# Optimization experiments

Measured on AMD Instinct MI355X. Metric: run time of the kernel, lower is better.

Reference implementation:

```python
import jax, jax.numpy as jnp
import numpy as np

B, D, S = 8, 128, 4096

def setup_inputs() -> dict:
    key = jax.random.key(0)
    ks = jax.random.split(key, 7)
    sd = 1.0 / np.sqrt(D)
    return {
        "x": jax.random.normal(ks[0], (B, D, S), dtype=jnp.float32),
        "Wq": jax.random.normal(ks[1], (D, D), dtype=jnp.float32) * sd,
        "bq": jax.random.normal(ks[2], (D,), dtype=jnp.float32) * sd,
        "Wk": jax.random.normal(ks[3], (D, D), dtype=jnp.float32) * sd,
        "bk": jax.random.normal(ks[4], (D,), dtype=jnp.float32) * sd,
        "Wv": jax.random.normal(ks[5], (D, D), dtype=jnp.float32) * sd,
        "bv": jax.random.normal(ks[6], (D,), dtype=jnp.float32) * sd,
    }

def reference(x, Wq, bq, Wk, bk, Wv, bv):
    # x: (B, D, S) -> (B, S, D)
    xt = jnp.transpose(x, (0, 2, 1))
    scale = jnp.asarray(D, xt.dtype) ** 0.5
    # torch Linear: y = x @ W.T + b
    Q = jnp.einsum('bsd,ed->bse', xt, Wq) + bq
    K = jnp.einsum('bsd,ed->bse', xt, Wk) + bk
    V = jnp.einsum('bsd,ed->bse', xt, Wv) + bv
    scores = jnp.einsum('bqd,bkd->bqk', Q, K) / scale  # (B, S, S)
    attn = jax.nn.softmax(scores, axis=-1)
    attended = jnp.einsum('bqk,bkd->bqd', attn, V)
    out = xt + attended  # residual
    return jnp.transpose(out, (0, 2, 1))  # back to (B, D, S)
```

## Files before the change

### kernel.cpp

```cpp
#include <hip/hip_runtime.h>
#include <hip/hip_bf16.h>

#define B_ 8
#define D_ 128
#define S_ 4096

typedef short short8 __attribute__((ext_vector_type(8)));
typedef float f32x4  __attribute__((ext_vector_type(4)));
typedef float f32x16 __attribute__((ext_vector_type(16)));
typedef unsigned int uint;
typedef uint uint4v __attribute__((ext_vector_type(4)));

#define EXP2F(x) exp2f(x)

__device__ __forceinline__ short f2bf(float f) {
    __hip_bfloat16 h = __float2bfloat16(f);
    return *reinterpret_cast<short*>(&h);
}

__device__ __forceinline__ uint cvtpk(float lo, float hi) {
    uint r;
    asm("v_cvt_pk_bf16_f32 %0, %1, %2" : "=v"(r) : "v"(lo), "v"(hi));
    return r;
}

__device__ __forceinline__ void gload16(const void* g, void* l) {
    __builtin_amdgcn_global_load_lds(
        (const __attribute__((address_space(1))) void*)g,
        (__attribute__((address_space(3))) void*)l, 16, 0, 0);
}

__global__ __launch_bounds__(256) void wpack_kernel(
    const float* __restrict__ Wq, const float* __restrict__ Wk,
    const float* __restrict__ Wv, short* __restrict__ Wf)
{
    int g = blockIdx.x * 256 + threadIdx.x;
    int lane = g & 63, kc = (g >> 6) & 3, n = (g >> 8) & 7, wm = g >> 11;
    const float* W = (wm == 0) ? Wq : (wm == 1) ? Wk : Wv;
    int row = n * 16 + (lane & 15);
    int col = kc * 32 + (lane >> 4) * 8;
    short8 o;
    #pragma unroll
    for (int j = 0; j < 8; ++j) o[j] = f2bf(W[row * 128 + col + j]);
    *((short8*)Wf + g) = o;
}

__global__ __launch_bounds__(256) void qkv_kernel(
    const float* __restrict__ x, const short* __restrict__ Wf,
    const float* __restrict__ bq, const float* __restrict__ bk,
    const float* __restrict__ bv,
    short* __restrict__ Qo, short* __restrict__ Ko, short* __restrict__ Vo)
{
    __shared__ float xt[64 * 132];
    const int b  = blockIdx.y;
    const int s0 = blockIdx.x * 64;
    const int t  = threadIdx.x;
    const int w    = t >> 6;
    const int lane = t & 63;
    const int lr   = lane & 15;
    const int lg   = lane >> 4;

    const float* xb = x + (size_t)b * D_ * S_;
    #pragma unroll
    for (int it = 0; it < 32; ++it) {
        int d = it * 4 + (t >> 6);
        int s = t & 63;
        xt[s * 132 + d] = xb[(size_t)d * S_ + s0 + s];
    }
    __syncthreads();

    short8 xtf[4];
    {
        const float* base = &xt[(w * 16 + lr) * 132 + lg * 8];
        #pragma unroll
        for (int kc = 0; kc < 4; ++kc) {
            float4 a = *(const float4*)(base + kc * 32);
            float4 c = *(const float4*)(base + kc * 32 + 4);
            short8 f;
            f[0] = f2bf(a.x); f[1] = f2bf(a.y); f[2] = f2bf(a.z); f[3] = f2bf(a.w);
            f[4] = f2bf(c.x); f[5] = f2bf(c.y); f[6] = f2bf(c.z); f[7] = f2bf(c.w);
            xtf[kc] = f;
        }
    }

    const float qs = 0.08838834764831845f * 1.4426950408889634f;
    const short8* W8 = (const short8*)Wf;
    const size_t bSD = (size_t)b * S_ * D_;
    const size_t bDS = (size_t)b * D_ * S_;

    #pragma unroll
    for (int n = 0; n < 8; ++n) {
        f32x4 aq = (f32x4){0.f, 0.f, 0.f, 0.f};
        f32x4 ak = (f32x4){0.f, 0.f, 0.f, 0.f};
        f32x4 av = (f32x4){0.f, 0.f, 0.f, 0.f};
        #pragma unroll
        for (int kc = 0; kc < 4; ++kc) {
            short8 wq = W8[(      n * 4 + kc) * 64 + lane];
            short8 wk = W8[(32  + n * 4 + kc) * 64 + lane];
            short8 wv = W8[(64  + n * 4 + kc) * 64 + lane];
            aq = __builtin_amdgcn_mfma_f32_16x16x32_bf16(xtf[kc], wq, aq, 0, 0, 0);
            ak = __builtin_amdgcn_mfma_f32_16x16x32_bf16(xtf[kc], wk, ak, 0, 0, 0);
            av = __builtin_amdgcn_mfma_f32_16x16x32_bf16(wv, xtf[kc], av, 0, 0, 0);
        }
        int e = n * 16 + lr;
        float bqe = bq[e], bke = bk[e];
        #pragma unroll
        for (int r = 0; r < 4; ++r) {
            size_t off = (bSD + (size_t)(s0 + w * 16 + lg * 4 + r) * D_) + e;
            Qo[off] = f2bf((aq[r] + bqe) * qs);
            Ko[off] = f2bf(ak[r] + bke);
        }
        #pragma unroll
        for (int r = 0; r < 4; ++r) {
            int ev = n * 16 + lg * 4 + r;
            Vo[bDS + (size_t)ev * S_ + s0 + w * 16 + lr] = f2bf(av[r] + bv[ev]);
        }
    }
}

__global__ __launch_bounds__(512, 2) void attn_kernel(
    const short* __restrict__ Q, const short* __restrict__ K,
    const short* __restrict__ Vt, const float* __restrict__ x,
    float* __restrict__ out)
{
    extern __shared__ __align__(16) char smem[];
    const int lin = blockIdx.x;
    const int b   = lin & 7;
    const int q0  = (lin >> 3) * 128;
    const int t    = threadIdx.x;
    const int w    = t >> 6;
    const int lane = t & 63;
    const int q    = lane & 31;
    const int hi   = lane >> 5;
    const int half = w >> 2;
    const int ww   = w & 3;

    const size_t bSD = (size_t)b * S_ * D_;

    short8 qf[8];
    {
        const short* Qrow = Q + bSD + (size_t)(q0 + ww * 32 + q) * D_ + hi * 8;
        #pragma unroll
        for (int c = 0; c < 8; ++c)
            qf[c] = *(const short8*)(Qrow + c * 16);
    }

    f32x16 o[4];
    #pragma unroll
    for (int dt = 0; dt < 4; ++dt)
        #pragma unroll
        for (int i = 0; i < 16; ++i) o[dt][i] = 0.f;
    float m = -1e30f, lsum = 0.f;

    const short* Kb = K + bSD;
    const short* Vb = Vt + (size_t)b * D_ * S_;
    const int ktbase = half * 32;

    auto stage = [&](int kt, int buf) {
        const short* Kg = Kb + (size_t)(ktbase + kt) * 64 * D_;
        const short* Vg = Vb + (size_t)(ktbase + kt) * 64;
        char* Kd = smem + buf * 65536 + half * 32768;
        char* Vd = Kd + 16384;
        #pragma unroll
        for (int i = 0; i < 4; ++i) {
            int ki = ww * 4 + i;
            int r  = ki * 4 + (lane >> 4);
            gload16(Kg + r * D_ + (((lane & 15) ^ (r & 7)) * 8), Kd + ki * 1024);
        }
        #pragma unroll
        for (int i = 0; i < 4; ++i) {
            int vi = ww * 4 + i;
            int r  = vi * 8 + (lane >> 3);
            gload16(Vg + (size_t)r * S_ + (((lane & 7) ^ (lane >> 3)) * 8),
                    Vd + vi * 1024);
        }
    };

    stage(0, 0);
    __syncthreads();
    int cur = 0;

    for (int kt = 0; kt < 32; ++kt) {
        if (kt + 1 < 32) stage(kt + 1, cur ^ 1);

        const char* Kh = smem + cur * 65536 + half * 32768;
        const char* Vh = Kh + 16384;

        f32x16 acc[2];
        #pragma unroll
        for (int n = 0; n < 2; ++n)
            #pragma unroll
            for (int i = 0; i < 16; ++i) acc[n][i] = 0.f;
        #pragma unroll
        for (int c = 0; c < 8; ++c) {
            #pragma unroll
            for (int n = 0; n < 2; ++n) {
                int row = n * 32 + q;
                short8 kf = *(const short8*)(Kh + row * 256
                              + (((c * 2 + hi) ^ (q & 7)) * 16));
                acc[n] = __builtin_amdgcn_mfma_f32_32x32x16_bf16(kf, qf[c], acc[n], 0, 0, 0);
            }
        }

        float tm = acc[0][0];
        #pragma unroll
        for (int n = 0; n < 2; ++n)
            #pragma unroll
            for (int r = 0; r < 16; ++r) tm = fmaxf(tm, acc[n][r]);
        tm = fmaxf(tm, __shfl_xor(tm, 32));
        if (!__all(tm <= m + 8.f)) {
            float mn   = fmaxf(m, tm);
            float corr = EXP2F(m - mn);
            m = mn; lsum *= corr;
            #pragma unroll
            for (int dt = 0; dt < 4; ++dt)
                #pragma unroll
                for (int r = 0; r < 16; ++r) o[dt][r] *= corr;
        }
        float ps = 0.f;
        #pragma unroll
        for (int n = 0; n < 2; ++n)
            #pragma unroll
            for (int r = 0; r < 16; ++r) {
                float e = EXP2F(acc[n][r] - m);
                acc[n][r] = e; ps += e;
            }
        ps += __shfl_xor(ps, 32);
        lsum += ps;

        short8 pf[4];
        #pragma unroll
        for (int kc = 0; kc < 4; ++kc) {
            int n = kc >> 1, c1 = (kc & 1) * 8;
            uint W0 = cvtpk(acc[n][c1 + 0], acc[n][c1 + 1]);
            uint W1 = cvtpk(acc[n][c1 + 2], acc[n][c1 + 3]);
            uint W2 = cvtpk(acc[n][c1 + 4], acc[n][c1 + 5]);
            uint W3 = cvtpk(acc[n][c1 + 6], acc[n][c1 + 7]);
            uint S0 = __shfl_xor(W0, 32);
            uint S1 = __shfl_xor(W1, 32);
            uint S2 = __shfl_xor(W2, 32);
            uint S3 = __shfl_xor(W3, 32);
            uint4v pw;
            pw.x = hi ? S2 : W0;
            pw.y = hi ? S3 : W1;
            pw.z = hi ? W2 : S0;
            pw.w = hi ? W3 : S1;
            pf[kc] = *reinterpret_cast<short8*>(&pw);
        }

        __builtin_amdgcn_s_setprio(1);
        #pragma unroll
        for (int kc = 0; kc < 4; ++kc) {
            #pragma unroll
            for (int dt = 0; dt < 4; ++dt) {
                int row = dt * 32 + q;
                short8 vf = *(const short8*)(Vh + row * 128
                              + (((kc * 2 + hi) ^ (q & 7)) * 16));
                o[dt] = __builtin_amdgcn_mfma_f32_32x32x16_bf16(vf, pf[kc], o[dt], 0, 0, 0);
            }
        }
        __builtin_amdgcn_s_setprio(0);

        __syncthreads();
        cur ^= 1;
    }

    if (half == 1) {
        float* obuf = (float*)(smem + ww * 16384);
        #pragma unroll
        for (int dt = 0; dt < 4; ++dt)
            #pragma unroll
            for (int r = 0; r < 16; ++r) {
                int dl = dt * 32 + (r & 3) + 8 * (r >> 2) + 4 * hi;
                obuf[dl * 32 + q] = o[dt][r];
            }
        if (hi == 0) {
            float* ml = (float*)(smem + 65536 + ww * 256);
            ml[q * 2]     = m;
            ml[q * 2 + 1] = lsum;
        }
    }
    __syncthreads();
    if (half == 0) {
        const float* obuf = (const float*)(smem + ww * 16384);
        const float* ml   = (const float*)(smem + 65536 + ww * 256);
        float m2 = ml[q * 2], l2 = ml[q * 2 + 1];
        float M  = fmaxf(m, m2);
        float c1 = EXP2F(m - M), c2 = EXP2F(m2 - M);
        float inv = 1.0f / (lsum * c1 + l2 * c2);
        const float* xb = x   + (size_t)b * D_ * S_;
        float*       ob = out + (size_t)b * D_ * S_;
        int s = q0 + ww * 32 + q;
        #pragma unroll
        for (int dt = 0; dt < 4; ++dt)
            #pragma unroll
            for (int r = 0; r < 16; ++r) {
                int dl = dt * 32 + (r & 3) + 8 * (r >> 2) + 4 * hi;
                float val = (o[dt][r] * c1 + obuf[dl * 32 + q] * c2) * inv;
                size_t g = (size_t)dl * S_ + s;
                ob[g] = xb[g] + val;
            }
    }
}

extern "C" void kernel_launch(void* const* d_in, const int* in_sizes, int n_in,
                              void* d_out, int out_size, void* d_ws, size_t ws_size,
                              hipStream_t stream) {
    const float* x  = (const float*)d_in[0];
    const float* Wq = (const float*)d_in[1];
    const float* bq = (const float*)d_in[2];
    const float* Wk = (const float*)d_in[3];
    const float* bk = (const float*)d_in[4];
    const float* Wv = (const float*)d_in[5];
    const float* bv = (const float*)d_in[6];
    float* out = (float*)d_out;

    size_t n = (size_t)B_ * S_ * D_;
    short* Qw = (short*)d_ws;
    short* Kw = Qw + n;
    short* Vw = Kw + n;
    short* Wf = (short*)d_out;

    wpack_kernel<<<24, 256, 0, stream>>>(Wq, Wk, Wv, Wf);

    dim3 grid(S_ / 64, B_);
    qkv_kernel<<<grid, 256, 0, stream>>>(x, Wf, bq, bk, bv, Qw, Kw, Vw);

    int smemB = 131072;
    (void)hipFuncSetAttribute((const void*)attn_kernel,
                              hipFuncAttributeMaxDynamicSharedMemorySize, smemB);
    attn_kernel<<<256, 512, smemB, stream>>>(Qw, Kw, Vw, x, out);
}
```

Measured before the change: 123.7 us.

## Split attention into 4-way KV partitions with smaller query tiles and direct V loads

Each block now handles 64 queries and splits the key range four ways across wave pairs, processing 32 keys per step instead of 64. V is read straight from global memory instead of being staged through LDS, which halves LDS use and raises the launch-bounds occupancy target. The P-fragment transpose uses v_permlane32_swap instead of shuffles. A four-way softmax merge runs through LDS at the end. The risks are uncoalesced global V reads, more synchronization per unit of work, and greater register pressure.

```diff
diff --git a/kernel.cpp b/kernel.cpp
--- a/kernel.cpp
+++ b/kernel.cpp
@@ -118,7 +118,7 @@
     }
 }
 
-__global__ __launch_bounds__(512, 2) void attn_kernel(
+__global__ __launch_bounds__(512, 4) void attn_kernel(
     const short* __restrict__ Q, const short* __restrict__ K,
     const short* __restrict__ Vt, const float* __restrict__ x,
     float* __restrict__ out)
@@ -126,14 +126,14 @@
     extern __shared__ __align__(16) char smem[];
     const int lin = blockIdx.x;
     const int b   = lin & 7;
-    const int q0  = (lin >> 3) * 128;
+    const int q0  = (lin >> 3) * 64;
     const int t    = threadIdx.x;
     const int w    = t >> 6;
     const int lane = t & 63;
     const int q    = lane & 31;
     const int hi   = lane >> 5;
-    const int half = w >> 2;
-    const int ww   = w & 3;
+    const int qr   = w >> 1;
+    const int ww   = w & 1;
 
     const size_t bSD = (size_t)b * S_ * D_;
 
@@ -154,26 +154,17 @@
 
     const short* Kb = K + bSD;
     const short* Vb = Vt + (size_t)b * D_ * S_;
-    const int ktbase = half * 32;
+    const int kvbase = qr * 1024;
 
     auto stage = [&](int kt, int buf) {
-        const short* Kg = Kb + (size_t)(ktbase + kt) * 64 * D_;
-        const short* Vg = Vb + (size_t)(ktbase + kt) * 64;
-        char* Kd = smem + buf * 65536 + half * 32768;
-        char* Vd = Kd + 16384;
+        const short* Kg = Kb + (size_t)(kvbase + kt * 32) * D_;
+        char* Kd = smem + buf * 32768 + qr * 8192;
         #pragma unroll
         for (int i = 0; i < 4; ++i) {
             int ki = ww * 4 + i;
             int r  = ki * 4 + (lane >> 4);
             gload16(Kg + r * D_ + (((lane & 15) ^ (r & 7)) * 8), Kd + ki * 1024);
         }
-        #pragma unroll
-        for (int i = 0; i < 4; ++i) {
-            int vi = ww * 4 + i;
-            int r  = vi * 8 + (lane >> 3);
-            gload16(Vg + (size_t)r * S_ + (((lane & 7) ^ (lane >> 3)) * 8),
-                    Vd + vi * 1024);
-        }
     };
 
     stage(0, 0);
@@ -183,30 +174,28 @@
     for (int kt = 0; kt < 32; ++kt) {
         if (kt + 1 < 32) stage(kt + 1, cur ^ 1);
 
-        const char* Kh = smem + cur * 65536 + half * 32768;
-        const char* Vh = Kh + 16384;
-
-        f32x16 acc[2];
-        #pragma unroll
-        for (int n = 0; n < 2; ++n)
-            #pragma unroll
-            for (int i = 0; i < 16; ++i) acc[n][i] = 0.f;
+        const char* Kh = smem + cur * 32768 + qr * 8192;
+
+        f32x16 acc;
+        #pragma unroll
+        for (int i = 0; i < 16; ++i) acc[i] = 0.f;
+        __builtin_amdgcn_s_setprio(1);
         #pragma unroll
         for (int c = 0; c < 8; ++c) {
-            #pragma unroll
-            for (int n = 0; n < 2; ++n) {
-                int row = n * 32 + q;
-                short8 kf = *(const short8*)(Kh + row * 256
-                              + (((c * 2 + hi) ^ (q & 7)) * 16));
-                acc[n] = __builtin_amdgcn_mfma_f32_32x32x16_bf16(kf, qf[c], acc[n], 0, 0, 0);
-            }
-        }
-
-        float tm = acc[0][0];
-        #pragma unroll
-        for (int n = 0; n < 2; ++n)
-            #pragma unroll
-            for (int r = 0; r < 16; ++r) tm = fmaxf(tm, acc[n][r]);
+            short8 kf = *(const short8*)(Kh + q * 256
+                          + (((c * 2 + hi) ^ (q & 7)) * 16));
+            acc = __builtin_amdgcn_mfma_f32_32x32x16_bf16(kf, qf[c], acc, 0, 0, 0);
+        }
+        __builtin_amdgcn_s_setprio(0);
+
+        float t0 = fmaxf(acc[0],  acc[1]),  t1 = fmaxf(acc[2],  acc[3]);
+        float t2 = fmaxf(acc[4],  acc[5]),  t3 = fmaxf(acc[6],  acc[7]);
+        float t4 = fmaxf(acc[8],  acc[9]),  t5 = fmaxf(acc[10], acc[11]);
+        float t6 = fmaxf(acc[12], acc[13]), t7 = fmaxf(acc[14], acc[15]);
+        float ta = fmaxf(fmaxf(t0, t1), t2);
+        float tb = fmaxf(fmaxf(t3, t4), t5);
+        float tc = fmaxf(t6, t7);
+        float tm = fmaxf(fmaxf(ta, tb), tc);
         tm = fmaxf(tm, __shfl_xor(tm, 32));
         if (!__all(tm <= m + 8.f)) {
             float mn   = fmaxf(m, tm);
@@ -217,77 +206,107 @@
                 #pragma unroll
                 for (int r = 0; r < 16; ++r) o[dt][r] *= corr;
         }
-        float ps = 0.f;
-        #pragma unroll
-        for (int n = 0; n < 2; ++n)
-            #pragma unroll
-            for (int r = 0; r < 16; ++r) {
-                float e = EXP2F(acc[n][r] - m);
-                acc[n][r] = e; ps += e;
-            }
+        #pragma unroll
+        for (int r = 0; r < 16; ++r) acc[r] = EXP2F(acc[r] - m);
+        float s0 = (acc[0] + acc[1]) + (acc[2] + acc[3]);
+        float s1 = (acc[4] + acc[5]) + (acc[6] + acc[7]);
+        float s2 = (acc[8] + acc[9]) + (acc[10] + acc[11]);
+        float s3 = (acc[12] + acc[13]) + (acc[14] + acc[15]);
+        float ps = (s0 + s1) + (s2 + s3);
         ps += __shfl_xor(ps, 32);
         lsum += ps;
 
-        short8 pf[4];
-        #pragma unroll
-        for (int kc = 0; kc < 4; ++kc) {
-            int n = kc >> 1, c1 = (kc & 1) * 8;
-            uint W0 = cvtpk(acc[n][c1 + 0], acc[n][c1 + 1]);
-            uint W1 = cvtpk(acc[n][c1 + 2], acc[n][c1 + 3]);
-            uint W2 = cvtpk(acc[n][c1 + 4], acc[n][c1 + 5]);
-            uint W3 = cvtpk(acc[n][c1 + 6], acc[n][c1 + 7]);
-            uint S0 = __shfl_xor(W0, 32);
-            uint S1 = __shfl_xor(W1, 32);
-            uint S2 = __shfl_xor(W2, 32);
-            uint S3 = __shfl_xor(W3, 32);
+        short8 pf[2];
+        #pragma unroll
+        for (int kc = 0; kc < 2; ++kc) {
+            int c1 = kc * 8;
+            uint W0 = cvtpk(acc[c1 + 0], acc[c1 + 1]);
+            uint W1 = cvtpk(acc[c1 + 2], acc[c1 + 3]);
+            uint W2 = cvtpk(acc[c1 + 4], acc[c1 + 5]);
+            uint W3 = cvtpk(acc[c1 + 6], acc[c1 + 7]);
+            asm("v_permlane32_swap_b32 %0, %1" : "+v"(W0), "+v"(W2));
+            asm("v_permlane32_swap_b32 %0, %1" : "+v"(W1), "+v"(W3));
             uint4v pw;
-            pw.x = hi ? S2 : W0;
-            pw.y = hi ? S3 : W1;
-            pw.z = hi ? W2 : S0;
-            pw.w = hi ? W3 : S1;
+            pw.x = W0;
+            pw.y = W1;
+            pw.z = W2;
+            pw.w = W3;
             pf[kc] = *reinterpret_cast<short8*>(&pw);
         }
 
+        const short* Vg = Vb + kvbase + kt * 32 + hi * 8;
         __builtin_amdgcn_s_setprio(1);
         #pragma unroll
-        for (int kc = 0; kc < 4; ++kc) {
+        for (int kc = 0; kc < 2; ++kc)
             #pragma unroll
             for (int dt = 0; dt < 4; ++dt) {
-                int row = dt * 32 + q;
-                short8 vf = *(const short8*)(Vh + row * 128
-                              + (((kc * 2 + hi) ^ (q & 7)) * 16));
+                short8 vf = *(const short8*)(Vg + (size_t)(dt * 32 + q) * S_
+                                             + kc * 16);
                 o[dt] = __builtin_amdgcn_mfma_f32_32x32x16_bf16(vf, pf[kc], o[dt], 0, 0, 0);
             }
-        }
         __builtin_amdgcn_s_setprio(0);
 
         __syncthreads();
         cur ^= 1;
     }
 
-    if (half == 1) {
-        float* obuf = (float*)(smem + ww * 16384);
+    float2* ml = (float2*)(smem + 65536);
+    if (hi == 0) {
+        float2 v2; v2.x = m; v2.y = lsum;
+        ml[(ww * 4 + qr) * 32 + q] = v2;
+    }
+    __syncthreads();
+    float M = -1e30f;
+    float mx[4], ly[4];
+    #pragma unroll
+    for (int i = 0; i < 4; ++i) {
+        float2 v2 = ml[(ww * 4 + i) * 32 + q];
+        mx[i] = v2.x; ly[i] = v2.y;
+        M = fmaxf(M, mx[i]);
+    }
+    float L = 0.f;
+    #pragma unroll
+    for (int i = 0; i < 4; ++i) L += ly[i] * EXP2F(mx[i] - M);
+    float cf = EXP2F(m - M);
+    #pragma unroll
+    for (int dt = 0; dt < 4; ++dt)
+        #pragma unroll
+        for (int r = 0; r < 16; ++r) o[dt][r] *= cf;
+
+    float* buf01 = (float*)smem + ww * 4096;
+    float* buf23 = (float*)smem + 8192 + ww * 4096;
+    if (qr == 1 || qr == 3) {
+        float* bw = (qr == 1) ? buf01 : buf23;
         #pragma unroll
         for (int dt = 0; dt < 4; ++dt)
             #pragma unroll
             for (int r = 0; r < 16; ++r) {
                 int dl = dt * 32 + (r & 3) + 8 * (r >> 2) + 4 * hi;
-                obuf[dl * 32 + q] = o[dt][r];
-            }
-        if (hi == 0) {
-            float* ml = (float*)(smem + 65536 + ww * 256);
-            ml[q * 2]     = m;
-            ml[q * 2 + 1] = lsum;
-        }
-    }
-    __syncthreads();
-    if (half == 0) {
-        const float* obuf = (const float*)(smem + ww * 16384);
-        const float* ml   = (const float*)(smem + 65536 + ww * 256);
-        float m2 = ml[q * 2], l2 = ml[q * 2 + 1];
-        float M  = fmaxf(m, m2);
-        float c1 = EXP2F(m - M), c2 = EXP2F(m2 - M);
-        float inv = 1.0f / (lsum * c1 + l2 * c2);
+                bw[dl * 32 + q] = o[dt][r];
+            }
+    }
+    __syncthreads();
+    if (qr == 0) {
+        #pragma unroll
+        for (int dt = 0; dt < 4; ++dt)
+            #pragma unroll
+            for (int r = 0; r < 16; ++r) {
+                int dl = dt * 32 + (r & 3) + 8 * (r >> 2) + 4 * hi;
+                o[dt][r] += buf01[dl * 32 + q];
+            }
+    } else if (qr == 2) {
+        #pragma unroll
+        for (int dt = 0; dt < 4; ++dt)
+            #pragma unroll
+            for (int r = 0; r < 16; ++r) {
+                int dl = dt * 32 + (r & 3) + 8 * (r >> 2) + 4 * hi;
+                o[dt][r] += buf23[dl * 32 + q];
+                buf23[dl * 32 + q] = o[dt][r];
+            }
+    }
+    __syncthreads();
+    if (qr == 0) {
+        float invL = 1.0f / L;
         const float* xb = x   + (size_t)b * D_ * S_;
         float*       ob = out + (size_t)b * D_ * S_;
         int s = q0 + ww * 32 + q;
@@ -296,7 +315,7 @@
             #pragma unroll
             for (int r = 0; r < 16; ++r) {
                 int dl = dt * 32 + (r & 3) + 8 * (r >> 2) + 4 * hi;
-                float val = (o[dt][r] * c1 + obuf[dl * 32 + q] * c2) * inv;
+                float val = (o[dt][r] + buf23[dl * 32 + q]) * invL;
                 size_t g = (size_t)dl * S_ + s;
                 ob[g] = xb[g] + val;
             }
@@ -326,8 +345,8 @@
     dim3 grid(S_ / 64, B_);
     qkv_kernel<<<grid, 256, 0, stream>>>(x, Wf, bq, bk, bv, Qw, Kw, Vw);
 
-    int smemB = 131072;
+    int smemB = 67584;
     (void)hipFuncSetAttribute((const void*)attn_kernel,
                               hipFuncAttributeMaxDynamicSharedMemorySize, smemB);
-    attn_kernel<<<256, 512, smemB, stream>>>(Qw, Kw, Vw, x, out);
-}
+    attn_kernel<<<512, 512, smemB, stream>>>(Qw, Kw, Vw, x, out);
+}
```

Result: slower. 268.6 us (+117.2%).

## Software-pipeline QK^T of next tile with softmax and PV of current tile

Applied to the files above, without the earlier changes.

Restructures the attention main loop so the QK^T MFMAs for tile t+1 are issued between the max reduction and the exponentials of tile t, using two ping-pong accumulator sets and an unrolled-by-two loop. K is now prefetched two tiles ahead and V one tile ahead, with a new shared-memory layout. The cross-half shuffle exchange is replaced by v_permlane32_swap, and the max/sum reductions become trees. The aim is to overlap matrix-core work with the exp/convert VALU work, at the cost of more live registers and possible spilling or lower occupancy.

```diff
diff --git a/kernel.cpp b/kernel.cpp
--- a/kernel.cpp
+++ b/kernel.cpp
@@ -127,9 +127,9 @@
     const int lin = blockIdx.x;
     const int b   = lin & 7;
     const int q0  = (lin >> 3) * 128;
-    const int t    = threadIdx.x;
-    const int w    = t >> 6;
-    const int lane = t & 63;
+    const int tid  = threadIdx.x;
+    const int w    = tid >> 6;
+    const int lane = tid & 63;
     const int q    = lane & 31;
     const int hi   = lane >> 5;
     const int half = w >> 2;
@@ -156,17 +156,22 @@
     const short* Vb = Vt + (size_t)b * D_ * S_;
     const int ktbase = half * 32;
 
-    auto stage = [&](int kt, int buf) {
+    char* const Kd0 = smem + half * 65536;
+    char* const Kd1 = Kd0 + 16384;
+    char* const Vd0 = Kd0 + 32768;
+    char* const Vd1 = Vd0 + 16384;
+
+    auto stageK = [&](int kt, char* Kd) {
         const short* Kg = Kb + (size_t)(ktbase + kt) * 64 * D_;
-        const short* Vg = Vb + (size_t)(ktbase + kt) * 64;
-        char* Kd = smem + buf * 65536 + half * 32768;
-        char* Vd = Kd + 16384;
         #pragma unroll
         for (int i = 0; i < 4; ++i) {
             int ki = ww * 4 + i;
             int r  = ki * 4 + (lane >> 4);
             gload16(Kg + r * D_ + (((lane & 15) ^ (r & 7)) * 8), Kd + ki * 1024);
         }
+    };
+    auto stageV = [&](int kt, char* Vd) {
+        const short* Vg = Vb + (size_t)(ktbase + kt) * 64;
         #pragma unroll
         for (int i = 0; i < 4; ++i) {
             int vi = ww * 4 + i;
@@ -176,37 +181,37 @@
         }
     };
 
-    stage(0, 0);
-    __syncthreads();
-    int cur = 0;
-
-    for (int kt = 0; kt < 32; ++kt) {
-        if (kt + 1 < 32) stage(kt + 1, cur ^ 1);
-
-        const char* Kh = smem + cur * 65536 + half * 32768;
-        const char* Vh = Kh + 16384;
-
-        f32x16 acc[2];
-        #pragma unroll
-        for (int n = 0; n < 2; ++n)
-            #pragma unroll
-            for (int i = 0; i < 16; ++i) acc[n][i] = 0.f;
+    auto qkrun = [&](const char* Kh, f32x16& a0, f32x16& a1) {
+        #pragma unroll
+        for (int i = 0; i < 16; ++i) { a0[i] = 0.f; a1[i] = 0.f; }
+        __builtin_amdgcn_s_setprio(1);
         #pragma unroll
         for (int c = 0; c < 8; ++c) {
-            #pragma unroll
-            for (int n = 0; n < 2; ++n) {
-                int row = n * 32 + q;
-                short8 kf = *(const short8*)(Kh + row * 256
-                              + (((c * 2 + hi) ^ (q & 7)) * 16));
-                acc[n] = __builtin_amdgcn_mfma_f32_32x32x16_bf16(kf, qf[c], acc[n], 0, 0, 0);
-            }
-        }
-
-        float tm = acc[0][0];
-        #pragma unroll
-        for (int n = 0; n < 2; ++n)
-            #pragma unroll
-            for (int r = 0; r < 16; ++r) tm = fmaxf(tm, acc[n][r]);
+            int co = ((c * 2 + hi) ^ (q & 7)) * 16;
+            short8 k0 = *(const short8*)(Kh + q * 256 + co);
+            short8 k1 = *(const short8*)(Kh + (32 + q) * 256 + co);
+            a0 = __builtin_amdgcn_mfma_f32_32x32x16_bf16(k0, qf[c], a0, 0, 0, 0);
+            a1 = __builtin_amdgcn_mfma_f32_32x32x16_bf16(k1, qf[c], a1, 0, 0, 0);
+        }
+        __builtin_amdgcn_s_setprio(0);
+    };
+
+    auto body = [&](int t, char* KstD, char* VstD, const char* Krd,
+                    const char* Vrd, f32x16& iA0, f32x16& iA1,
+                    f32x16& oB0, f32x16& oB1) {
+        if (t + 2 < 32) stageK(t + 2, KstD);
+        if (t + 1 < 32) stageV(t + 1, VstD);
+
+        float x0 = fmaxf(fmaxf(iA0[0],  iA0[1]),  fmaxf(iA0[2],  iA0[3]));
+        float x1 = fmaxf(fmaxf(iA0[4],  iA0[5]),  fmaxf(iA0[6],  iA0[7]));
+        float x2 = fmaxf(fmaxf(iA0[8],  iA0[9]),  fmaxf(iA0[10], iA0[11]));
+        float x3 = fmaxf(fmaxf(iA0[12], iA0[13]), fmaxf(iA0[14], iA0[15]));
+        float x4 = fmaxf(fmaxf(iA1[0],  iA1[1]),  fmaxf(iA1[2],  iA1[3]));
+        float x5 = fmaxf(fmaxf(iA1[4],  iA1[5]),  fmaxf(iA1[6],  iA1[7]));
+        float x6 = fmaxf(fmaxf(iA1[8],  iA1[9]),  fmaxf(iA1[10], iA1[11]));
+        float x7 = fmaxf(fmaxf(iA1[12], iA1[13]), fmaxf(iA1[14], iA1[15]));
+        float tm = fmaxf(fmaxf(fmaxf(x0, x1), fmaxf(x2, x3)),
+                         fmaxf(fmaxf(x4, x5), fmaxf(x6, x7)));
         tm = fmaxf(tm, __shfl_xor(tm, 32));
         if (!__all(tm <= m + 8.f)) {
             float mn   = fmaxf(m, tm);
@@ -217,52 +222,67 @@
                 #pragma unroll
                 for (int r = 0; r < 16; ++r) o[dt][r] *= corr;
         }
-        float ps = 0.f;
-        #pragma unroll
-        for (int n = 0; n < 2; ++n)
-            #pragma unroll
-            for (int r = 0; r < 16; ++r) {
-                float e = EXP2F(acc[n][r] - m);
-                acc[n][r] = e; ps += e;
-            }
+
+        if (t + 1 < 32) qkrun(Krd, oB0, oB1);
+
+        #pragma unroll
+        for (int r = 0; r < 16; ++r) iA0[r] = EXP2F(iA0[r] - m);
+        #pragma unroll
+        for (int r = 0; r < 16; ++r) iA1[r] = EXP2F(iA1[r] - m);
+        float s0 = ((iA0[0]+iA0[1])+(iA0[2]+iA0[3]))
+                 + ((iA0[4]+iA0[5])+(iA0[6]+iA0[7]));
+        float s1 = ((iA0[8]+iA0[9])+(iA0[10]+iA0[11]))
+                 + ((iA0[12]+iA0[13])+(iA0[14]+iA0[15]));
+        float s2 = ((iA1[0]+iA1[1])+(iA1[2]+iA1[3]))
+                 + ((iA1[4]+iA1[5])+(iA1[6]+iA1[7]));
+        float s3 = ((iA1[8]+iA1[9])+(iA1[10]+iA1[11]))
+                 + ((iA1[12]+iA1[13])+(iA1[14]+iA1[15]));
+        float ps = (s0 + s1) + (s2 + s3);
         ps += __shfl_xor(ps, 32);
         lsum += ps;
 
         short8 pf[4];
         #pragma unroll
         for (int kc = 0; kc < 4; ++kc) {
-            int n = kc >> 1, c1 = (kc & 1) * 8;
-            uint W0 = cvtpk(acc[n][c1 + 0], acc[n][c1 + 1]);
-            uint W1 = cvtpk(acc[n][c1 + 2], acc[n][c1 + 3]);
-            uint W2 = cvtpk(acc[n][c1 + 4], acc[n][c1 + 5]);
-            uint W3 = cvtpk(acc[n][c1 + 6], acc[n][c1 + 7]);
-            uint S0 = __shfl_xor(W0, 32);
-            uint S1 = __shfl_xor(W1, 32);
-            uint S2 = __shfl_xor(W2, 32);
-            uint S3 = __shfl_xor(W3, 32);
+            const f32x16& a = (kc < 2) ? iA0 : iA1;
+            int c1 = (kc & 1) * 8;
+            uint W0 = cvtpk(a[c1 + 0], a[c1 + 1]);
+            uint W1 = cvtpk(a[c1 + 2], a[c1 + 3]);
+            uint W2 = cvtpk(a[c1 + 4], a[c1 + 5]);
+            uint W3 = cvtpk(a[c1 + 6], a[c1 + 7]);
+            asm("v_permlane32_swap_b32 %0, %1" : "+v"(W0), "+v"(W2));
+            asm("v_permlane32_swap_b32 %0, %1" : "+v"(W1), "+v"(W3));
             uint4v pw;
-            pw.x = hi ? S2 : W0;
-            pw.y = hi ? S3 : W1;
-            pw.z = hi ? W2 : S0;
-            pw.w = hi ? W3 : S1;
+            pw.x = W0; pw.y = W1; pw.z = W2; pw.w = W3;
             pf[kc] = *reinterpret_cast<short8*>(&pw);
         }
 
         __builtin_amdgcn_s_setprio(1);
         #pragma unroll
-        for (int kc = 0; kc < 4; ++kc) {
+        for (int kc = 0; kc < 4; ++kc)
             #pragma unroll
             for (int dt = 0; dt < 4; ++dt) {
                 int row = dt * 32 + q;
-                short8 vf = *(const short8*)(Vh + row * 128
+                short8 vf = *(const short8*)(Vrd + row * 128
                               + (((kc * 2 + hi) ^ (q & 7)) * 16));
                 o[dt] = __builtin_amdgcn_mfma_f32_32x32x16_bf16(vf, pf[kc], o[dt], 0, 0, 0);
             }
-        }
         __builtin_amdgcn_s_setprio(0);
 
         __syncthreads();
-        cur ^= 1;
+    };
+
+    stageK(0, Kd0); stageV(0, Vd0); stageK(1, Kd1);
+    __syncthreads();
+    f32x16 aA0, aA1, aB0, aB1;
+    #pragma unroll
+    for (int i = 0; i < 16; ++i) { aB0[i] = 0.f; aB1[i] = 0.f; }
+    qkrun(Kd0, aA0, aA1);
+    __syncthreads();
+
+    for (int t = 0; t < 32; t += 2) {
+        body(t,     Kd0, Vd1, Kd1, Vd0, aA0, aA1, aB0, aB1);
+        body(t + 1, Kd1, Vd0, Kd0, Vd1, aB0, aB1, aA0, aA1);
     }
 
     if (half == 1) {
```

New measurement: 123.8 us. Within noise of the previous version (+0.1%).

## Split attention tile into two halves and interleave softmax with MFMA

Applied to the files above, without the earlier changes.

Restructures the inner loop so each 64-key tile is processed as two 32-key halves. The max/exp/pack of one half is scheduled alongside the QK or PV MFMAs of the other, with sched_group_barrier hints and software-pipelined LDS fragment loads. The cross-half shuffle for the P fragment is replaced by v_permlane32_swap, max and sum use tree reductions, and the per-tile lsum shuffle is deferred to after the loop. This aims to hide VALU softmax work under matrix-core work, at the cost of an extra rescale gate per half and more register pressure.

```diff
diff --git a/kernel.cpp b/kernel.cpp
--- a/kernel.cpp
+++ b/kernel.cpp
@@ -28,6 +28,10 @@
     __builtin_amdgcn_global_load_lds(
         (const __attribute__((address_space(1))) void*)g,
         (__attribute__((address_space(3))) void*)l, 16, 0, 0);
+}
+
+__device__ __forceinline__ float max3f(float a, float b, float c) {
+    return fmaxf(fmaxf(a, b), c);
 }
 
 __global__ __launch_bounds__(256) void wpack_kernel(
@@ -127,9 +131,9 @@
     const int lin = blockIdx.x;
     const int b   = lin & 7;
     const int q0  = (lin >> 3) * 128;
-    const int t    = threadIdx.x;
-    const int w    = t >> 6;
-    const int lane = t & 63;
+    const int tid  = threadIdx.x;
+    const int w    = tid >> 6;
+    const int lane = tid & 63;
     const int q    = lane & 31;
     const int hi   = lane >> 5;
     const int half = w >> 2;
@@ -176,38 +180,7 @@
         }
     };
 
-    stage(0, 0);
-    __syncthreads();
-    int cur = 0;
-
-    for (int kt = 0; kt < 32; ++kt) {
-        if (kt + 1 < 32) stage(kt + 1, cur ^ 1);
-
-        const char* Kh = smem + cur * 65536 + half * 32768;
-        const char* Vh = Kh + 16384;
-
-        f32x16 acc[2];
-        #pragma unroll
-        for (int n = 0; n < 2; ++n)
-            #pragma unroll
-            for (int i = 0; i < 16; ++i) acc[n][i] = 0.f;
-        #pragma unroll
-        for (int c = 0; c < 8; ++c) {
-            #pragma unroll
-            for (int n = 0; n < 2; ++n) {
-                int row = n * 32 + q;
-                short8 kf = *(const short8*)(Kh + row * 256
-                              + (((c * 2 + hi) ^ (q & 7)) * 16));
-                acc[n] = __builtin_amdgcn_mfma_f32_32x32x16_bf16(kf, qf[c], acc[n], 0, 0, 0);
-            }
-        }
-
-        float tm = acc[0][0];
-        #pragma unroll
-        for (int n = 0; n < 2; ++n)
-            #pragma unroll
-            for (int r = 0; r < 16; ++r) tm = fmaxf(tm, acc[n][r]);
-        tm = fmaxf(tm, __shfl_xor(tm, 32));
+    auto gate = [&](float tm) {
         if (!__all(tm <= m + 8.f)) {
             float mn   = fmaxf(m, tm);
             float corr = EXP2F(m - mn);
@@ -217,53 +190,159 @@
                 #pragma unroll
                 for (int r = 0; r < 16; ++r) o[dt][r] *= corr;
         }
-        float ps = 0.f;
-        #pragma unroll
-        for (int n = 0; n < 2; ++n)
-            #pragma unroll
-            for (int r = 0; r < 16; ++r) {
-                float e = EXP2F(acc[n][r] - m);
-                acc[n][r] = e; ps += e;
-            }
-        ps += __shfl_xor(ps, 32);
-        lsum += ps;
-
-        short8 pf[4];
-        #pragma unroll
-        for (int kc = 0; kc < 4; ++kc) {
-            int n = kc >> 1, c1 = (kc & 1) * 8;
-            uint W0 = cvtpk(acc[n][c1 + 0], acc[n][c1 + 1]);
-            uint W1 = cvtpk(acc[n][c1 + 2], acc[n][c1 + 3]);
-            uint W2 = cvtpk(acc[n][c1 + 4], acc[n][c1 + 5]);
-            uint W3 = cvtpk(acc[n][c1 + 6], acc[n][c1 + 7]);
-            uint S0 = __shfl_xor(W0, 32);
-            uint S1 = __shfl_xor(W1, 32);
-            uint S2 = __shfl_xor(W2, 32);
-            uint S3 = __shfl_xor(W3, 32);
+    };
+    auto exppack = [&](f32x16& A, short8* pf) {
+        #pragma unroll
+        for (int r = 0; r < 16; ++r) A[r] = EXP2F(A[r] - m);
+        #pragma unroll
+        for (int kc = 0; kc < 2; ++kc) {
+            int c1 = kc * 8;
+            uint W0 = cvtpk(A[c1 + 0], A[c1 + 1]);
+            uint W1 = cvtpk(A[c1 + 2], A[c1 + 3]);
+            uint W2 = cvtpk(A[c1 + 4], A[c1 + 5]);
+            uint W3 = cvtpk(A[c1 + 6], A[c1 + 7]);
+            asm("v_permlane32_swap_b32 %0, %1" : "+v"(W0), "+v"(W2));
+            asm("v_permlane32_swap_b32 %0, %1" : "+v"(W1), "+v"(W3));
             uint4v pw;
-            pw.x = hi ? S2 : W0;
-            pw.y = hi ? S3 : W1;
-            pw.z = hi ? W2 : S0;
-            pw.w = hi ? W3 : S1;
+            pw.x = W0; pw.y = W1; pw.z = W2; pw.w = W3;
             pf[kc] = *reinterpret_cast<short8*>(&pw);
         }
-
+    };
+    auto tree16 = [&](const f32x16& A) -> float {
+        float x0 = max3f(A[0],  A[1],  A[2]);
+        float x1 = max3f(A[3],  A[4],  A[5]);
+        float x2 = max3f(A[6],  A[7],  A[8]);
+        float x3 = max3f(A[9],  A[10], A[11]);
+        float x4 = max3f(A[12], A[13], A[14]);
+        float y0 = max3f(x0, x1, x2);
+        float y1 = max3f(x3, x4, A[15]);
+        return fmaxf(y0, y1);
+    };
+    auto sum16 = [&](const f32x16& A) -> float {
+        float s0 = ((A[0]+A[1])+(A[2]+A[3])) + ((A[4]+A[5])+(A[6]+A[7]));
+        float s1 = ((A[8]+A[9])+(A[10]+A[11])) + ((A[12]+A[13])+(A[14]+A[15]));
+        return s0 + s1;
+    };
+
+    stage(0, 0);
+    __syncthreads();
+    int cur = 0;
+
+    for (int kt = 0; kt < 32; ++kt) {
+        if (kt + 1 < 32) stage(kt + 1, cur ^ 1);
+
+        const char* Kh = smem + cur * 65536 + half * 32768;
+        const char* Vh = Kh + 16384;
+
+        f32x16 acc0, acc1;
+        #pragma unroll
+        for (int i = 0; i < 16; ++i) acc0[i] = 0.f;
+        short8 kf[3];
+        {
+            int co0 = ((0 + hi) ^ (q & 7)) * 16;
+            int co1 = ((2 + hi) ^ (q & 7)) * 16;
+            kf[0] = *(const short8*)(Kh + q * 256 + co0);
+            kf[1] = *(const short8*)(Kh + q * 256 + co1);
+        }
+        #pragma unroll
+        for (int c = 0; c < 8; ++c) {
+            if (c < 6) {
+                int co = (((c + 2) * 2 + hi) ^ (q & 7)) * 16;
+                kf[(c + 2) % 3] = *(const short8*)(Kh + q * 256 + co);
+            }
+            acc0 = __builtin_amdgcn_mfma_f32_32x32x16_bf16(kf[c % 3], qf[c], acc0, 0, 0, 0);
+        }
+
+        #pragma unroll
+        for (int i = 0; i < 16; ++i) acc1[i] = 0.f;
+        short8 kg[3];
+        {
+            int co0 = ((0 + hi) ^ (q & 7)) * 16;
+            int co1 = ((2 + hi) ^ (q & 7)) * 16;
+            kg[0] = *(const short8*)(Kh + (32 + q) * 256 + co0);
+            kg[1] = *(const short8*)(Kh + (32 + q) * 256 + co1);
+        }
+        #pragma unroll
+        for (int c = 0; c < 8; ++c) {
+            if (c < 6) {
+                int co = (((c + 2) * 2 + hi) ^ (q & 7)) * 16;
+                kg[(c + 2) % 3] = *(const short8*)(Kh + (32 + q) * 256 + co);
+            }
+            acc1 = __builtin_amdgcn_mfma_f32_32x32x16_bf16(kg[c % 3], qf[c], acc1, 0, 0, 0);
+        }
+        float tm0 = tree16(acc0);
+        #pragma unroll
+        for (int g = 0; g < 6; ++g) {
+            __builtin_amdgcn_sched_group_barrier(0x100, 1, 0);
+            __builtin_amdgcn_sched_group_barrier(0x008, 1, 0);
+            __builtin_amdgcn_sched_group_barrier(0x002, 2, 0);
+        }
+        __builtin_amdgcn_sched_group_barrier(0x008, 1, 0);
+        __builtin_amdgcn_sched_group_barrier(0x002, 2, 0);
+        __builtin_amdgcn_sched_group_barrier(0x008, 1, 0);
+
+        tm0 = fmaxf(tm0, __shfl_xor(tm0, 32));
+        gate(tm0);
+        short8 pf0[2];
+        exppack(acc0, pf0);
+
+        short8 vf[3];
+        {
+            int co0 = ((0 + hi) ^ (q & 7)) * 16;
+            vf[0] = *(const short8*)(Vh + (0 * 32 + q) * 128 + co0);
+            vf[1] = *(const short8*)(Vh + (1 * 32 + q) * 128 + co0);
+        }
+        #pragma unroll
+        for (int i = 0; i < 8; ++i) {
+            if (i < 6) {
+                int j  = i + 2;
+                int co = (((j >> 2) * 2 + hi) ^ (q & 7)) * 16;
+                vf[j % 3] = *(const short8*)(Vh + ((j & 3) * 32 + q) * 128 + co);
+            }
+            o[i & 3] = __builtin_amdgcn_mfma_f32_32x32x16_bf16(
+                vf[i % 3], pf0[i >> 2], o[i & 3], 0, 0, 0);
+        }
+        float tm1 = tree16(acc1);
+        lsum += sum16(acc0);
+        #pragma unroll
+        for (int g = 0; g < 6; ++g) {
+            __builtin_amdgcn_sched_group_barrier(0x100, 1, 0);
+            __builtin_amdgcn_sched_group_barrier(0x008, 1, 0);
+            __builtin_amdgcn_sched_group_barrier(0x002, 4, 0);
+        }
+        __builtin_amdgcn_sched_group_barrier(0x008, 1, 0);
+        __builtin_amdgcn_sched_group_barrier(0x002, 2, 0);
+        __builtin_amdgcn_sched_group_barrier(0x008, 1, 0);
+
+        tm1 = fmaxf(tm1, __shfl_xor(tm1, 32));
+        gate(tm1);
+        short8 pf1[2];
+        exppack(acc1, pf1);
+
+        {
+            int co2 = ((4 + hi) ^ (q & 7)) * 16;
+            vf[0] = *(const short8*)(Vh + (0 * 32 + q) * 128 + co2);
+            vf[1] = *(const short8*)(Vh + (1 * 32 + q) * 128 + co2);
+        }
+        lsum += sum16(acc1);
         __builtin_amdgcn_s_setprio(1);
         #pragma unroll
-        for (int kc = 0; kc < 4; ++kc) {
-            #pragma unroll
-            for (int dt = 0; dt < 4; ++dt) {
-                int row = dt * 32 + q;
-                short8 vf = *(const short8*)(Vh + row * 128
-                              + (((kc * 2 + hi) ^ (q & 7)) * 16));
-                o[dt] = __builtin_amdgcn_mfma_f32_32x32x16_bf16(vf, pf[kc], o[dt], 0, 0, 0);
-            }
+        for (int i = 0; i < 8; ++i) {
+            if (i < 6) {
+                int j  = i + 2;
+                int co = ((((j >> 2) + 2) * 2 + hi) ^ (q & 7)) * 16;
+                vf[j % 3] = *(const short8*)(Vh + ((j & 3) * 32 + q) * 128 + co);
+            }
+            o[i & 3] = __builtin_amdgcn_mfma_f32_32x32x16_bf16(
+                vf[i % 3], pf1[i >> 2], o[i & 3], 0, 0, 0);
         }
         __builtin_amdgcn_s_setprio(0);
 
         __syncthreads();
         cur ^= 1;
     }
+
+    lsum += __shfl_xor(lsum, 32);
 
     if (half == 1) {
         float* obuf = (float*)(smem + ww * 16384);
```

Measured after the change: 121.0 us. 2.1% less time.
